# Kernel tuning notes

Measured on AMD Instinct MI355X. Metric: run time of the kernel, lower is better.

The kernel has to match this reference:

```python
import jax, jax.numpy as jnp
import numpy as np

MIN_V = -20.0
MAX_V = 20.0
NUM_BINS = 255          # support has NUM_BINS+1 = 256 points
N = 131072              # number of target elements / rows of logits
C = NUM_BINS + 1


def setup_inputs() -> dict:
    key = jax.random.key(0)
    k1, k2 = jax.random.split(key)
    logits = jax.random.normal(k1, (N, C), dtype=jnp.float32)
    # targets strictly inside (min, max) so the two-hot index is in [1, NUM_BINS]
    target = jax.random.uniform(k2, (N,), dtype=jnp.float32,
                                minval=MIN_V + 0.05, maxval=MAX_V - 0.05)
    return {"logits": logits, "target": target}


def _two_hot_probs(target):
    # support = linspace(min, max, num_bins+1)
    support = jnp.linspace(MIN_V, MAX_V, C, dtype=jnp.float32)
    # idx = number of support points strictly below target (== torch (support < t).sum())
    idx = jnp.searchsorted(support, target, side='left')          # [N] in [1, NUM_BINS]
    lo = support[idx - 1]                                         # support[idx-1]
    hi = support[idx]                                             # support[idx]
    delta = hi - lo
    w_lo = jnp.abs(hi - target) / delta    # weight placed at bin idx-1
    w_hi = jnp.abs(lo - target) / delta    # weight placed at bin idx
    rows = jnp.arange(target.shape[0])
    probs = jnp.zeros((target.shape[0], C), dtype=jnp.float32)
    probs = probs.at[rows, idx - 1].set(w_lo).at[rows, idx].set(w_hi)
    return probs


def reference(logits, target):
    probs = _two_hot_probs(target)                  # [N, C] soft labels
    logp = jax.nn.log_softmax(logits, axis=-1)      # [N, C]
    # F.cross_entropy with soft targets: mean over batch of -sum(p * log_softmax)
    return -jnp.mean(jnp.sum(probs * logp, axis=-1))
```

## Files before the change

### kernel.cpp

```cpp
#include <hip/hip_runtime.h>


#define NCOLS 256

__global__ __launch_bounds__(256, 8) void twohot_ce_kernel(
    const float* __restrict__ logits, const float* __restrict__ target,
    float* __restrict__ out, int nrows)
{
    const int lane = threadIdx.x & 63;
    const int wid  = threadIdx.x >> 6;
    const int q    = lane & 15;
    const int sub  = lane >> 4;

    const int gwave  = blockIdx.x * 4 + wid;
    const int nwaves = gridDim.x * 4;

    const float inv_delta = 255.0f / 40.0f;
    const float qf = (float)(q << 2);

    float acc = 0.0f;

    for (int base = gwave * 4; base < nrows; base += nwaves * 4) {
        const int row = base + sub;
        const float4* rp = reinterpret_cast<const float4*>(
            logits + (size_t)row * NCOLS);

        const float4 x0 = rp[q];
        const float4 x1 = rp[q + 16];
        const float4 x2 = rp[q + 32];
        const float4 x3 = rp[q + 48];

        const float t = target[row];
        const float u = (t + 20.0f) * inv_delta;
        const float g = qf - u;

        float s = 0.0f, d = 0.0f;
        const float4 xs[4] = {x0, x1, x2, x3};
        #pragma unroll
        for (int j = 0; j < 4; ++j) {
            const float vx[4] = {xs[j].x, xs[j].y, xs[j].z, xs[j].w};
            #pragma unroll
            for (int k = 0; k < 4; ++k) {
                const float xv = vx[k];
                s += __expf(xv);
                const float a = g + (float)(j * 64 + k);
                const float w = fmaxf(1.0f - fabsf(a), 0.0f);
                d = fmaf(w, xv, d);
            }
        }

        #pragma unroll
        for (int o = 1; o < 16; o <<= 1) {
            s += __shfl_xor(s, o, 64);
            d += __shfl_xor(d, o, 64);
        }

        acc += __logf(s) - d;
    }

    acc += __shfl_xor(acc, 16, 64);
    acc += __shfl_xor(acc, 32, 64);

    __shared__ float wave_acc[4];
    if (lane == 0) wave_acc[wid] = acc;
    __syncthreads();
    if (threadIdx.x == 0) {
        const float tot = wave_acc[0] + wave_acc[1] + wave_acc[2] + wave_acc[3];
        atomicAdd(out, tot / (float)nrows);
    }
}

extern "C" void kernel_launch(void* const* d_in, const int* in_sizes, int n_in,
                              void* d_out, int out_size, void* d_ws, size_t ws_size,
                              hipStream_t stream) {
    const float* logits = (const float*)d_in[0];
    const float* target = (const float*)d_in[1];
    float* out = (float*)d_out;
    const int nrows = in_sizes[1];

    hipMemsetAsync(out, 0, sizeof(float), stream);

    twohot_ce_kernel<<<dim3(2048), dim3(256), 0, stream>>>(logits, target, out, nrows);
}
```

Measured before the change: 193.1 us.

## Restructure to half-wave rows with double-buffered loads and per-block row tiles

Each half-wave now processes one row with two float4 loads per lane, and the next row's loads are issued before computing the current one through explicit double buffering. The grid becomes nrows/64 blocks, each covering a fixed 64-row tile, instead of a grid-stride loop over 2048 blocks, and a separate tail kernel handles leftover rows. This aims to keep more memory requests in flight and hide latency, at the cost of more registers, a longer shuffle reduction, and many more blocks each issuing its own atomic.

```diff
diff --git a/kernel.cpp b/kernel.cpp
--- a/kernel.cpp
+++ b/kernel.cpp
@@ -2,6 +2,47 @@
 
 
 #define NCOLS 256
+
+struct B2 {
+    float4 a0, a1;
+    float  t;
+};
+
+__device__ __forceinline__ B2 load2(const float* __restrict__ logits,
+                                    const float* __restrict__ target,
+                                    int row, int h)
+{
+    B2 b;
+    const float4* rp = reinterpret_cast<const float4*>(logits + (size_t)row * NCOLS);
+    b.a0 = rp[h];
+    b.a1 = rp[h + 32];
+    b.t  = target[row];
+    return b;
+}
+
+__device__ __forceinline__ float comp2(const B2& b, float c0)
+{
+    const float inv_delta = 255.0f / 40.0f;
+    const float u = (b.t + 20.0f) * inv_delta;
+    float s = 0.0f, d = 0.0f;
+    const float v0[4] = {b.a0.x, b.a0.y, b.a0.z, b.a0.w};
+    const float v1[4] = {b.a1.x, b.a1.y, b.a1.z, b.a1.w};
+    #pragma unroll
+    for (int k = 0; k < 4; ++k) {
+        s += __expf(v0[k]);
+        float w = fmaxf(1.0f - fabsf(c0 + (float)k - u), 0.0f);
+        d = fmaf(w, v0[k], d);
+        s += __expf(v1[k]);
+        w = fmaxf(1.0f - fabsf(c0 + (float)(128 + k) - u), 0.0f);
+        d = fmaf(w, v1[k], d);
+    }
+    #pragma unroll
+    for (int o = 1; o < 32; o <<= 1) {
+        s += __shfl_xor(s, o, 64);
+        d += __shfl_xor(d, o, 64);
+    }
+    return __logf(s) - d;
+}
 
 __global__ __launch_bounds__(256, 8) void twohot_ce_kernel(
     const float* __restrict__ logits, const float* __restrict__ target,
@@ -9,56 +50,25 @@
 {
     const int lane = threadIdx.x & 63;
     const int wid  = threadIdx.x >> 6;
-    const int q    = lane & 15;
-    const int sub  = lane >> 4;
+    const int h    = lane & 31;
+    const int half = lane >> 5;
+    const float c0 = (float)(h << 2);
 
-    const int gwave  = blockIdx.x * 4 + wid;
-    const int nwaves = gridDim.x * 4;
-
-    const float inv_delta = 255.0f / 40.0f;
-    const float qf = (float)(q << 2);
+    const int wrow0 = blockIdx.x * 64 + wid * 16 + half;
 
     float acc = 0.0f;
 
-    for (int base = gwave * 4; base < nrows; base += nwaves * 4) {
-        const int row = base + sub;
-        const float4* rp = reinterpret_cast<const float4*>(
-            logits + (size_t)row * NCOLS);
+    B2 A  = load2(logits, target, wrow0 + 0, h);
+    B2 Bb = load2(logits, target, wrow0 + 2, h);
 
-        const float4 x0 = rp[q];
-        const float4 x1 = rp[q + 16];
-        const float4 x2 = rp[q + 32];
-        const float4 x3 = rp[q + 48];
-
-        const float t = target[row];
-        const float u = (t + 20.0f) * inv_delta;
-        const float g = qf - u;
-
-        float s = 0.0f, d = 0.0f;
-        const float4 xs[4] = {x0, x1, x2, x3};
-        #pragma unroll
-        for (int j = 0; j < 4; ++j) {
-            const float vx[4] = {xs[j].x, xs[j].y, xs[j].z, xs[j].w};
-            #pragma unroll
-            for (int k = 0; k < 4; ++k) {
-                const float xv = vx[k];
-                s += __expf(xv);
-                const float a = g + (float)(j * 64 + k);
-                const float w = fmaxf(1.0f - fabsf(a), 0.0f);
-                d = fmaf(w, xv, d);
-            }
-        }
-
-        #pragma unroll
-        for (int o = 1; o < 16; o <<= 1) {
-            s += __shfl_xor(s, o, 64);
-            d += __shfl_xor(d, o, 64);
-        }
-
-        acc += __logf(s) - d;
+    #pragma unroll 1
+    for (int b = 0; b < 8; b += 2) {
+        acc += comp2(A, c0);
+        if (b + 2 < 8) A  = load2(logits, target, wrow0 + (b + 2) * 2, h);
+        acc += comp2(Bb, c0);
+        if (b + 3 < 8) Bb = load2(logits, target, wrow0 + (b + 3) * 2, h);
     }
 
-    acc += __shfl_xor(acc, 16, 64);
     acc += __shfl_xor(acc, 32, 64);
 
     __shared__ float wave_acc[4];
@@ -68,6 +78,33 @@
         const float tot = wave_acc[0] + wave_acc[1] + wave_acc[2] + wave_acc[3];
         atomicAdd(out, tot / (float)nrows);
     }
+}
+
+__global__ __launch_bounds__(64) void twohot_ce_tail(
+    const float* __restrict__ logits, const float* __restrict__ target,
+    float* __restrict__ out, int row0, int nrows)
+{
+    const int row = row0 + blockIdx.x;
+    if (row >= nrows) return;
+    const int lane = threadIdx.x;
+    const float4 x = reinterpret_cast<const float4*>(logits + (size_t)row * NCOLS)[lane];
+    const float inv_delta = 255.0f / 40.0f;
+    const float u = (target[row] + 20.0f) * inv_delta;
+    const float c0 = (float)(lane << 2);
+    float s = 0.0f, d = 0.0f;
+    const float v[4] = {x.x, x.y, x.z, x.w};
+    #pragma unroll
+    for (int k = 0; k < 4; ++k) {
+        s += __expf(v[k]);
+        const float w = fmaxf(1.0f - fabsf(c0 + (float)k - u), 0.0f);
+        d = fmaf(w, v[k], d);
+    }
+    #pragma unroll
+    for (int o = 1; o < 64; o <<= 1) {
+        s += __shfl_xor(s, o, 64);
+        d += __shfl_xor(d, o, 64);
+    }
+    if (lane == 0) atomicAdd(out, (__logf(s) - d) / (float)nrows);
 }
 
 extern "C" void kernel_launch(void* const* d_in, const int* in_sizes, int n_in,
@@ -80,5 +117,12 @@
 
     hipMemsetAsync(out, 0, sizeof(float), stream);
 
-    twohot_ce_kernel<<<dim3(2048), dim3(256), 0, stream>>>(logits, target, out, nrows);
+    const int nblocks = nrows / 64;
+    if (nblocks > 0)
+        twohot_ce_kernel<<<dim3(nblocks), dim3(256), 0, stream>>>(
+            logits, target, out, nrows);
+    const int rem = nrows - nblocks * 64;
+    if (rem > 0)
+        twohot_ce_tail<<<dim3(rem), dim3(64), 0, stream>>>(
+            logits, target, out, nblocks * 64, nrows);
 }
```

Result: slower. 201.1 us (+4.1%).
